# Kernel tuning notes

Hardware: AMD Instinct MI355X
Metric: run time of the kernel (lower is better)

## Reference

```python
import jax, jax.numpy as jnp
import numpy as np


def setup_inputs() -> dict:
    key = jax.random.key(0)
    ks = jax.random.split(key, 5)
    B, N, H, S, D = 1, 256, 4, 256, 32
    q = jax.random.normal(ks[0], (B, N, H, S, D), dtype=jnp.float32)
    k = jax.random.normal(ks[1], (B, N, H, S, D), dtype=jnp.float32)
    v = jax.random.normal(ks[2], (B, N, H, S, D), dtype=jnp.float32)
    mask_bias = jax.random.normal(ks[3], (B, N, 1, 1, S), dtype=jnp.float32)
    triangle_bias = jax.random.normal(ks[4], (B, 1, H, S, S), dtype=jnp.float32)
    return {"q": q, "k": k, "v": v, "mask_bias": mask_bias, "triangle_bias": triangle_bias}


def reference(q, k, v, mask_bias, triangle_bias):
    # q,k,v: [B, N, H, S, D]; mask_bias: [B, N, 1, 1, S]; triangle_bias: [B, 1, H, S, S]
    D = q.shape[-1]
    sm_scale = 1.0 / jnp.sqrt(jnp.asarray(D, dtype=q.dtype))
    # scores: [B, N, H, S, S] (query index s attends over key index t)
    scores = jnp.einsum("bnhsd,bnhtd->bnhst", q, k) * sm_scale
    scores = scores + mask_bias + triangle_bias  # broadcast add of both biases
    p = jax.nn.softmax(scores, axis=-1)
    out = jnp.einsum("bnhst,bnhtd->bnhsd", p, v)
    return out
```

## Files before the change

### kernel.cpp

```cpp
#include <hip/hip_runtime.h>

typedef __bf16 bf16;
typedef bf16 bf16x8 __attribute__((ext_vector_type(8)));
typedef bf16 bf16x4 __attribute__((ext_vector_type(4)));
typedef float f32x4 __attribute__((ext_vector_type(4)));

#define SEQ 256
#define DH  32
#define VT_PAD 264
#define P_PAD  40

__global__ __launch_bounds__(256, 4) void attn_mfma_kernel(
    const float* __restrict__ q,
    const float* __restrict__ k,
    const float* __restrict__ v,
    const float* __restrict__ mask_bias,
    const float* __restrict__ tri_bias,
    float* __restrict__ out)
{
    __shared__ bf16 Vt[DH][VT_PAD];
    __shared__ bf16 Pb[4][64][P_PAD];

    const int tid  = threadIdx.x;
    const int wave = tid >> 6;
    const int lane = tid & 63;
    const int l15  = lane & 15;
    const int quad = lane >> 4;

    const int inst = blockIdx.x;
    const int n    = inst >> 2;
    const int h    = inst & 3;

    const float* qb = q + (size_t)inst * SEQ * DH;
    const float* kb = k + (size_t)inst * SEQ * DH;
    const float* vb = v + (size_t)inst * SEQ * DH;
    const float* mb = mask_bias + (size_t)n * SEQ;
    const float* tb = tri_bias + (size_t)h * SEQ * SEQ;

    const float K1    = 0.17677669529663687f * 1.44269504088896f;
    const float LOG2E = 1.44269504088896f;

    #pragma unroll
    for (int i = 0; i < 8; ++i) {
        int idx = i * 256 + tid;
        int t = idx >> 3;
        int d = (idx & 7) * 4;
        float4 tv = ((const float4*)vb)[idx];
        Vt[d + 0][t] = (bf16)tv.x;
        Vt[d + 1][t] = (bf16)tv.y;
        Vt[d + 2][t] = (bf16)tv.z;
        Vt[d + 3][t] = (bf16)tv.w;
    }
    __syncthreads();

    const int s_base = wave * 64;
    bf16x8 qfrag[4];
    #pragma unroll
    for (int st = 0; st < 4; ++st) {
        const float* p = qb + (size_t)(s_base + st * 16 + l15) * DH + quad * 8;
        float4 a = ((const float4*)p)[0];
        float4 b = ((const float4*)p)[1];
        bf16x8 f;
        f[0] = (bf16)a.x; f[1] = (bf16)a.y; f[2] = (bf16)a.z; f[3] = (bf16)a.w;
        f[4] = (bf16)b.x; f[5] = (bf16)b.y; f[6] = (bf16)b.z; f[7] = (bf16)b.w;
        qfrag[st] = f;
    }

    f32x4 oacc[4][2];
    #pragma unroll
    for (int st = 0; st < 4; ++st)
        #pragma unroll
        for (int dt = 0; dt < 2; ++dt)
            oacc[st][dt] = (f32x4){0.f, 0.f, 0.f, 0.f};
    float lpart[4] = {0.f, 0.f, 0.f, 0.f};

    const f32x4 zero4 = {0.f, 0.f, 0.f, 0.f};

    for (int c = 0; c < 8; ++c) {
        #pragma unroll
        for (int half = 0; half < 2; ++half) {
            const int mt = c * 2 + half;
            const int t0 = mt * 16;

            const float* kp = kb + (size_t)(t0 + l15) * DH + quad * 8;
            float4 ka = ((const float4*)kp)[0];
            float4 kc = ((const float4*)kp)[1];
            bf16x8 kfrag;
            kfrag[0] = (bf16)ka.x; kfrag[1] = (bf16)ka.y;
            kfrag[2] = (bf16)ka.z; kfrag[3] = (bf16)ka.w;
            kfrag[4] = (bf16)kc.x; kfrag[5] = (bf16)kc.y;
            kfrag[6] = (bf16)kc.z; kfrag[7] = (bf16)kc.w;

            float4 mk = *(const float4*)(mb + t0 + quad * 4);
            float4 tr[4];
            #pragma unroll
            for (int st = 0; st < 4; ++st) {
                const float* tp = tb + (size_t)(s_base + st * 16 + l15) * SEQ + t0 + quad * 4;
                tr[st] = *(const float4*)tp;
            }
            float mkl0 = mk.x * LOG2E, mkl1 = mk.y * LOG2E;
            float mkl2 = mk.z * LOG2E, mkl3 = mk.w * LOG2E;

            f32x4 cf[4];
            #pragma unroll
            for (int st = 0; st < 4; ++st)
                cf[st] = __builtin_amdgcn_mfma_f32_16x16x32_bf16(kfrag, qfrag[st], zero4, 0, 0, 0);

            #pragma unroll
            for (int st = 0; st < 4; ++st) {
                float p0 = __builtin_amdgcn_exp2f(fmaf(tr[st].x, LOG2E, fmaf(cf[st][0], K1, mkl0)));
                float p1 = __builtin_amdgcn_exp2f(fmaf(tr[st].y, LOG2E, fmaf(cf[st][1], K1, mkl1)));
                float p2 = __builtin_amdgcn_exp2f(fmaf(tr[st].z, LOG2E, fmaf(cf[st][2], K1, mkl2)));
                float p3 = __builtin_amdgcn_exp2f(fmaf(tr[st].w, LOG2E, fmaf(cf[st][3], K1, mkl3)));
                lpart[st] += (p0 + p1) + (p2 + p3);
                bf16x4 pk;
                pk[0] = (bf16)p0; pk[1] = (bf16)p1; pk[2] = (bf16)p2; pk[3] = (bf16)p3;
                *(bf16x4*)&Pb[wave][st * 16 + l15][half * 16 + quad * 4] = pk;
            }
        }

        bf16x8 vf[2];
        #pragma unroll
        for (int dt = 0; dt < 2; ++dt)
            vf[dt] = *(const bf16x8*)&Vt[dt * 16 + l15][c * 32 + quad * 8];
        #pragma unroll
        for (int st = 0; st < 4; ++st) {
            bf16x8 pf = *(const bf16x8*)&Pb[wave][st * 16 + l15][quad * 8];
            #pragma unroll
            for (int dt = 0; dt < 2; ++dt)
                oacc[st][dt] = __builtin_amdgcn_mfma_f32_16x16x32_bf16(pf, vf[dt], oacc[st][dt], 0, 0, 0);
        }
    }

    float linv[4];
    #pragma unroll
    for (int st = 0; st < 4; ++st) {
        float x = lpart[st];
        x += __shfl_xor(x, 16);
        x += __shfl_xor(x, 32);
        linv[st] = 1.0f / x;
    }

    float* ob = out + (size_t)inst * SEQ * DH;
    #pragma unroll
    for (int st = 0; st < 4; ++st) {
        #pragma unroll
        for (int r = 0; r < 4; ++r) {
            float invr = __shfl(linv[st], quad * 4 + r);
            int s = s_base + st * 16 + quad * 4 + r;
            float* orow = ob + (size_t)s * DH;
            orow[l15]      = oacc[st][0][r] * invr;
            orow[16 + l15] = oacc[st][1][r] * invr;
        }
    }
}

extern "C" void kernel_launch(void* const* d_in, const int* in_sizes, int n_in,
                              void* d_out, int out_size, void* d_ws, size_t ws_size,
                              hipStream_t stream) {
    const float* q    = (const float*)d_in[0];
    const float* k    = (const float*)d_in[1];
    const float* v    = (const float*)d_in[2];
    const float* mask = (const float*)d_in[3];
    const float* tri  = (const float*)d_in[4];
    float* out = (float*)d_out;

    attn_mfma_kernel<<<dim3(256 * 4), dim3(256), 0, stream>>>(q, k, v, mask, tri, out);
}
```

Measured before the change: 178.2 us.

## Split query rows across two blocks, XCD-aware mapping, prefetch K and bias tiles

Each (n,h) instance is now handled by two blocks, each covering 128 query rows, so the grid doubles to 2048 blocks and each wave owns 32 rows instead of 64. Block indices are remapped so that blocks on the same XCD share a head and reuse its triangle bias in L2. K and triangle-bias loads for the next chunk are software-prefetched into registers, and the mask is staged in shared memory. The cost is that each block recomputes the V transpose and reads K twice per instance, in exchange for more parallelism, higher occupancy (launch bound 5) and hidden load latency.

```diff
diff --git a/kernel.cpp b/kernel.cpp
--- a/kernel.cpp
+++ b/kernel.cpp
@@ -7,10 +7,10 @@
 
 #define SEQ 256
 #define DH  32
-#define VT_PAD 264
-#define P_PAD  40
+#define VROW 264
+#define PROW 40
 
-__global__ __launch_bounds__(256, 4) void attn_mfma_kernel(
+__global__ __launch_bounds__(256, 5) void attn_mfma4_kernel(
     const float* __restrict__ q,
     const float* __restrict__ k,
     const float* __restrict__ v,
@@ -18,8 +18,9 @@
     const float* __restrict__ tri_bias,
     float* __restrict__ out)
 {
-    __shared__ bf16 Vt[DH][VT_PAD];
-    __shared__ bf16 Pb[4][64][P_PAD];
+    __shared__ bf16  Vt[DH][VROW];
+    __shared__ bf16  Pb[4][32][PROW];
+    __shared__ float Mc[SEQ];
 
     const int tid  = threadIdx.x;
     const int wave = tid >> 6;
@@ -27,127 +28,137 @@
     const int l15  = lane & 15;
     const int quad = lane >> 4;
 
-    const int inst = blockIdx.x;
-    const int n    = inst >> 2;
-    const int h    = inst & 3;
+    const int b     = blockIdx.x;
+    const int xcd   = b & 7;
+    const int j     = b >> 3;
+    const int h     = xcd & 3;
+    const int n     = (j >> 1) + ((xcd >> 2) << 7);
+    const int qhalf = j & 1;
+    const int inst  = n * 4 + h;
 
     const float* qb = q + (size_t)inst * SEQ * DH;
     const float* kb = k + (size_t)inst * SEQ * DH;
     const float* vb = v + (size_t)inst * SEQ * DH;
     const float* mb = mask_bias + (size_t)n * SEQ;
     const float* tb = tri_bias + (size_t)h * SEQ * SEQ;
+    float*       ob = out + (size_t)inst * SEQ * DH;
+
+    const int s0 = qhalf * 128 + wave * 32;
 
     const float K1    = 0.17677669529663687f * 1.44269504088896f;
     const float LOG2E = 1.44269504088896f;
+    const f32x4 zero4 = {0.f, 0.f, 0.f, 0.f};
 
     #pragma unroll
     for (int i = 0; i < 8; ++i) {
         int idx = i * 256 + tid;
         int t = idx >> 3;
         int d = (idx & 7) * 4;
-        float4 tv = ((const float4*)vb)[idx];
-        Vt[d + 0][t] = (bf16)tv.x;
-        Vt[d + 1][t] = (bf16)tv.y;
-        Vt[d + 2][t] = (bf16)tv.z;
-        Vt[d + 3][t] = (bf16)tv.w;
+        float4 fv = ((const float4*)vb)[idx];
+        Vt[d + 0][t] = (bf16)fv.x;
+        Vt[d + 1][t] = (bf16)fv.y;
+        Vt[d + 2][t] = (bf16)fv.z;
+        Vt[d + 3][t] = (bf16)fv.w;
     }
-    __syncthreads();
+    Mc[tid] = mb[tid];
 
-    const int s_base = wave * 64;
-    bf16x8 qfrag[4];
+    bf16x8 qfrag[2];
     #pragma unroll
-    for (int st = 0; st < 4; ++st) {
-        const float* p = qb + (size_t)(s_base + st * 16 + l15) * DH + quad * 8;
+    for (int st = 0; st < 2; ++st) {
+        const float* p = qb + (size_t)(s0 + st * 16 + l15) * DH + quad * 8;
         float4 a = ((const float4*)p)[0];
-        float4 b = ((const float4*)p)[1];
+        float4 c4 = ((const float4*)p)[1];
         bf16x8 f;
-        f[0] = (bf16)a.x; f[1] = (bf16)a.y; f[2] = (bf16)a.z; f[3] = (bf16)a.w;
-        f[4] = (bf16)b.x; f[5] = (bf16)b.y; f[6] = (bf16)b.z; f[7] = (bf16)b.w;
+        f[0]=(bf16)a.x;  f[1]=(bf16)a.y;  f[2]=(bf16)a.z;  f[3]=(bf16)a.w;
+        f[4]=(bf16)c4.x; f[5]=(bf16)c4.y; f[6]=(bf16)c4.z; f[7]=(bf16)c4.w;
         qfrag[st] = f;
     }
 
-    f32x4 oacc[4][2];
+    const float* trp0 = tb + (size_t)(s0 + l15) * SEQ;
+    const float* trp1 = tb + (size_t)(s0 + 16 + l15) * SEQ;
+    float4 t00 = *(const float4*)(trp0 + quad * 4);
+    float4 t01 = *(const float4*)(trp1 + quad * 4);
+    float4 t10 = *(const float4*)(trp0 + 16 + quad * 4);
+    float4 t11 = *(const float4*)(trp1 + 16 + quad * 4);
+    float4 k0a = *(const float4*)(kb + (l15) * DH + quad * 8);
+    float4 k0b = *(const float4*)(kb + (l15) * DH + quad * 8 + 4);
+    float4 k1a = *(const float4*)(kb + (16 + l15) * DH + quad * 8);
+    float4 k1b = *(const float4*)(kb + (16 + l15) * DH + quad * 8 + 4);
+
+    __syncthreads();
+
+    f32x4 oacc[2][2];
     #pragma unroll
-    for (int st = 0; st < 4; ++st)
+    for (int st = 0; st < 2; ++st)
         #pragma unroll
         for (int dt = 0; dt < 2; ++dt)
-            oacc[st][dt] = (f32x4){0.f, 0.f, 0.f, 0.f};
-    float lpart[4] = {0.f, 0.f, 0.f, 0.f};
-
-    const f32x4 zero4 = {0.f, 0.f, 0.f, 0.f};
+            oacc[st][dt] = zero4;
+    float lpart[2] = {0.f, 0.f};
 
     for (int c = 0; c < 8; ++c) {
         #pragma unroll
         for (int half = 0; half < 2; ++half) {
-            const int mt = c * 2 + half;
-            const int t0 = mt * 16;
+            float4 ka = half ? k1a : k0a;
+            float4 kc = half ? k1b : k0b;
+            bf16x8 kfrag;
+            kfrag[0]=(bf16)ka.x; kfrag[1]=(bf16)ka.y; kfrag[2]=(bf16)ka.z; kfrag[3]=(bf16)ka.w;
+            kfrag[4]=(bf16)kc.x; kfrag[5]=(bf16)kc.y; kfrag[6]=(bf16)kc.z; kfrag[7]=(bf16)kc.w;
 
-            const float* kp = kb + (size_t)(t0 + l15) * DH + quad * 8;
-            float4 ka = ((const float4*)kp)[0];
-            float4 kc = ((const float4*)kp)[1];
-            bf16x8 kfrag;
-            kfrag[0] = (bf16)ka.x; kfrag[1] = (bf16)ka.y;
-            kfrag[2] = (bf16)ka.z; kfrag[3] = (bf16)ka.w;
-            kfrag[4] = (bf16)kc.x; kfrag[5] = (bf16)kc.y;
-            kfrag[6] = (bf16)kc.z; kfrag[7] = (bf16)kc.w;
-
-            float4 mk = *(const float4*)(mb + t0 + quad * 4);
-            float4 tr[4];
-            #pragma unroll
-            for (int st = 0; st < 4; ++st) {
-                const float* tp = tb + (size_t)(s_base + st * 16 + l15) * SEQ + t0 + quad * 4;
-                tr[st] = *(const float4*)tp;
-            }
+            float4 mk = *(const float4*)&Mc[c * 32 + half * 16 + quad * 4];
             float mkl0 = mk.x * LOG2E, mkl1 = mk.y * LOG2E;
             float mkl2 = mk.z * LOG2E, mkl3 = mk.w * LOG2E;
 
-            f32x4 cf[4];
             #pragma unroll
-            for (int st = 0; st < 4; ++st)
-                cf[st] = __builtin_amdgcn_mfma_f32_16x16x32_bf16(kfrag, qfrag[st], zero4, 0, 0, 0);
-
-            #pragma unroll
-            for (int st = 0; st < 4; ++st) {
-                float p0 = __builtin_amdgcn_exp2f(fmaf(tr[st].x, LOG2E, fmaf(cf[st][0], K1, mkl0)));
-                float p1 = __builtin_amdgcn_exp2f(fmaf(tr[st].y, LOG2E, fmaf(cf[st][1], K1, mkl1)));
-                float p2 = __builtin_amdgcn_exp2f(fmaf(tr[st].z, LOG2E, fmaf(cf[st][2], K1, mkl2)));
-                float p3 = __builtin_amdgcn_exp2f(fmaf(tr[st].w, LOG2E, fmaf(cf[st][3], K1, mkl3)));
-                lpart[st] += (p0 + p1) + (p2 + p3);
-                bf16x4 pk;
-                pk[0] = (bf16)p0; pk[1] = (bf16)p1; pk[2] = (bf16)p2; pk[3] = (bf16)p3;
+            for (int st = 0; st < 2; ++st) {
+                float4 tr = half ? (st ? t11 : t10) : (st ? t01 : t00);
+                f32x4 cf = __builtin_amdgcn_mfma_f32_16x16x32_bf16(kfrag, qfrag[st], zero4, 0, 0, 0);
+                float e0 = __builtin_amdgcn_exp2f(fmaf(cf[0], K1, fmaf(tr.x, LOG2E, mkl0)));
+                float e1 = __builtin_amdgcn_exp2f(fmaf(cf[1], K1, fmaf(tr.y, LOG2E, mkl1)));
+                float e2 = __builtin_amdgcn_exp2f(fmaf(cf[2], K1, fmaf(tr.z, LOG2E, mkl2)));
+                float e3 = __builtin_amdgcn_exp2f(fmaf(cf[3], K1, fmaf(tr.w, LOG2E, mkl3)));
+                lpart[st] += (e0 + e1) + (e2 + e3);
+                bf16x4 pk; pk[0]=(bf16)e0; pk[1]=(bf16)e1; pk[2]=(bf16)e2; pk[3]=(bf16)e3;
                 *(bf16x4*)&Pb[wave][st * 16 + l15][half * 16 + quad * 4] = pk;
             }
         }
 
-        bf16x8 vf[2];
+        {
+            const int cn = (c + 1) & 7;
+            t00 = *(const float4*)(trp0 + cn * 32 + quad * 4);
+            t01 = *(const float4*)(trp1 + cn * 32 + quad * 4);
+            t10 = *(const float4*)(trp0 + cn * 32 + 16 + quad * 4);
+            t11 = *(const float4*)(trp1 + cn * 32 + 16 + quad * 4);
+            k0a = *(const float4*)(kb + (cn * 32 + l15) * DH + quad * 8);
+            k0b = *(const float4*)(kb + (cn * 32 + l15) * DH + quad * 8 + 4);
+            k1a = *(const float4*)(kb + (cn * 32 + 16 + l15) * DH + quad * 8);
+            k1b = *(const float4*)(kb + (cn * 32 + 16 + l15) * DH + quad * 8 + 4);
+        }
+
+        bf16x8 vf0 = *(const bf16x8*)&Vt[l15][c * 32 + quad * 8];
+        bf16x8 vf1 = *(const bf16x8*)&Vt[16 + l15][c * 32 + quad * 8];
         #pragma unroll
-        for (int dt = 0; dt < 2; ++dt)
-            vf[dt] = *(const bf16x8*)&Vt[dt * 16 + l15][c * 32 + quad * 8];
-        #pragma unroll
-        for (int st = 0; st < 4; ++st) {
+        for (int st = 0; st < 2; ++st) {
             bf16x8 pf = *(const bf16x8*)&Pb[wave][st * 16 + l15][quad * 8];
-            #pragma unroll
-            for (int dt = 0; dt < 2; ++dt)
-                oacc[st][dt] = __builtin_amdgcn_mfma_f32_16x16x32_bf16(pf, vf[dt], oacc[st][dt], 0, 0, 0);
+            oacc[st][0] = __builtin_amdgcn_mfma_f32_16x16x32_bf16(pf, vf0, oacc[st][0], 0, 0, 0);
+            oacc[st][1] = __builtin_amdgcn_mfma_f32_16x16x32_bf16(pf, vf1, oacc[st][1], 0, 0, 0);
         }
     }
 
-    float linv[4];
+    float linv[2];
     #pragma unroll
-    for (int st = 0; st < 4; ++st) {
+    for (int st = 0; st < 2; ++st) {
         float x = lpart[st];
         x += __shfl_xor(x, 16);
         x += __shfl_xor(x, 32);
         linv[st] = 1.0f / x;
     }
 
-    float* ob = out + (size_t)inst * SEQ * DH;
     #pragma unroll
-    for (int st = 0; st < 4; ++st) {
+    for (int st = 0; st < 2; ++st) {
         #pragma unroll
         for (int r = 0; r < 4; ++r) {
             float invr = __shfl(linv[st], quad * 4 + r);
-            int s = s_base + st * 16 + quad * 4 + r;
+            int s = s0 + st * 16 + quad * 4 + r;
             float* orow = ob + (size_t)s * DH;
             orow[l15]      = oacc[st][0][r] * invr;
             orow[16 + l15] = oacc[st][1][r] * invr;
@@ -165,5 +176,5 @@
     const float* tri  = (const float*)d_in[4];
     float* out = (float*)d_out;
 
-    attn_mfma_kernel<<<dim3(256 * 4), dim3(256), 0, stream>>>(q, k, v, mask, tri, out);
+    attn_mfma4_kernel<<<dim3(2048), dim3(256), 0, stream>>>(q, k, v, mask, tri, out);
 }
```

Measured after the change: 186.8 us. 1.05x slower.
